# Kernel tuning notes

Measured on AMD Instinct MI355X. Metric: run time of the kernel, lower is better.

## Reference

```python
import jax, jax.numpy as jnp
import numpy as np
from jax import lax

B, NPG = 128, 1024          # graphs, nodes per graph
N = B * NPG                  # total nodes
AVG_DEG = 8
E = N * AVG_DEG              # total edges
F_N, F_E = 128, 32           # node / edge feature dims
LATENT = [32, 32, 32, 1]
D = sum(LATENT)              # total_latent_dim = 97
K = 30                       # sort-pooling k
C1, C2, KW2 = 16, 32, 5      # conv1d channels / kernel
OUT = 2
DENSE = ((K - 2) // 2 + 1 - KW2 + 1) * C2  # 352


def setup_inputs() -> dict:
    key = jax.random.key(0)
    ks = jax.random.split(key, 12)
    inp = {}
    inp["node_feat"] = jax.random.normal(ks[0], (N, F_N), jnp.float32)
    inp["edge_feat"] = jax.random.normal(ks[1], (E, F_E), jnp.float32)
    inp["edge_index"] = jax.random.randint(ks[2], (2, E), 0, N)
    dims = [F_N + F_E] + LATENT
    for i in range(4):
        inp[f"W{i}"] = jax.random.normal(ks[3 + i], (dims[i], dims[i + 1]), jnp.float32) * 0.05
        inp[f"b{i}"] = jnp.zeros((dims[i + 1],), jnp.float32)
    inp["w_conv1"] = jax.random.normal(ks[7], (C1, 1, D), jnp.float32) * 0.05
    inp["b_conv1"] = jnp.zeros((C1,), jnp.float32)
    inp["w_conv2"] = jax.random.normal(ks[8], (C2, C1, KW2), jnp.float32) * 0.05
    inp["b_conv2"] = jnp.zeros((C2,), jnp.float32)
    inp["w_out"] = jax.random.normal(ks[9], (DENSE, OUT), jnp.float32) * 0.05
    inp["b_out"] = jnp.zeros((OUT,), jnp.float32)
    return inp


def _maxpool2(x):
    # MaxPool1d(2, 2) over last axis of [B, C, L]
    return lax.reduce_window(x, -jnp.inf, lax.max, (1, 1, 2), (1, 1, 2), "VALID")


def _forward(node_feat, edge_feat, W0, b0, W1, b1, W2, b2, W3, b3,
             w_conv1, b_conv1, w_conv2, b_conv2, w_out, b_out, edge_index):
    src, dst = edge_index[0], edge_index[1]
    # degree with self-loop, as in DGCNN (divide by deg after linear)
    deg = jnp.ones((N,), node_feat.dtype).at[dst].add(1.0)
    # e2npool: sum incident edge features onto destination nodes
    e2n = jax.ops.segment_sum(edge_feat, dst, num_segments=N)
    cur = jnp.concatenate([node_feat, e2n], axis=1)  # [N, F_N+F_E]
    hops = []
    for W, b in ((W0, b0), (W1, b1), (W2, b2), (W3, b3)):
        # (A + I) X  -> Linear -> / deg -> tanh
        pooled = jax.ops.segment_sum(cur[src], dst, num_segments=N) + cur
        cur = jnp.tanh((pooled @ W + b) / deg[:, None])
        hops.append(cur)
    feat = jnp.concatenate(hops, axis=1).reshape(B, NPG, D)  # [B, NPG, 97]
    # SortPooling: top-k nodes per graph by last latent channel
    _, idx = lax.top_k(feat[:, :, -1], K)                    # [B, K]
    sp = jnp.take_along_axis(feat, idx[:, :, None], axis=1)  # [B, K, D]
    x = sp.reshape(B, 1, K * D)
    x = lax.conv_general_dilated(x, w_conv1, (D,), "VALID",
                                 dimension_numbers=("NCH", "OIH", "NCH"))
    x = jax.nn.relu(x + b_conv1[None, :, None])  # [B, 16, 30]
    x = _maxpool2(x)                              # [B, 16, 15]
    x = lax.conv_general_dilated(x, w_conv2, (1,), "VALID",
                                 dimension_numbers=("NCH", "OIH", "NCH"))
    x = jax.nn.relu(x + b_conv2[None, :, None])  # [B, 32, 11]
    x = x.reshape(B, -1)                          # [B, 352]
    return jax.nn.relu(x @ w_out + b_out)         # [B, OUT]


def reference(node_feat, edge_feat, edge_index, W0, b0, W1, b1, W2, b2, W3, b3,
              w_conv1, b_conv1, w_conv2, b_conv2, w_out, b_out):
    return _forward(node_feat, edge_feat, W0, b0, W1, b1, W2, b2, W3, b3,
                    w_conv1, b_conv1, w_conv2, b_conv2, w_out, b_out, edge_index)
```

## Files before the change

### kernel.cpp

```cpp
#include <hip/hip_runtime.h>
#include <hip/hip_bf16.h>
#include <math.h>

#define N_NODES 131072
#define N_EDGES 1048576
#define B_GR    128
#define NPG_    1024
#define KTOP    30


__global__ __launch_bounds__(256) void k_zero(int* cnt) {
    int i = blockIdx.x * 256 + threadIdx.x;
    if (i < N_NODES) cnt[i] = 0;
}

__global__ __launch_bounds__(256) void k_count(const int* __restrict__ dst, int* __restrict__ cnt) {
    int xcd = blockIdx.x & 7;
    int base = (blockIdx.x >> 3) * 4096 + threadIdx.x;
    #pragma unroll
    for (int it = 0; it < 16; ++it) {
        int e = base + it * 256;
        int d = __builtin_nontemporal_load(dst + e);
        if ((d >> 14) == xcd) atomicAdd(&cnt[d], 1);
    }
}

__global__ __launch_bounds__(256) void k_scan1(const int* __restrict__ cnt,
                                               int* __restrict__ row_start,
                                               int* __restrict__ blocksum) {
    __shared__ int s[256];
    int t = threadIdx.x;
    int i = blockIdx.x * 256 + t;
    int v = cnt[i];
    s[t] = v; __syncthreads();
    for (int o = 1; o < 256; o <<= 1) {
        int x = (t >= o) ? s[t - o] : 0;
        __syncthreads();
        s[t] += x;
        __syncthreads();
    }
    row_start[i] = s[t] - v;
    if (t == 255) blocksum[blockIdx.x] = s[t];
}

__global__ __launch_bounds__(512) void k_scan2(int* __restrict__ blocksum) {
    __shared__ int s[512];
    int t = threadIdx.x;
    int v = blocksum[t];
    s[t] = v; __syncthreads();
    for (int o = 1; o < 512; o <<= 1) {
        int x = (t >= o) ? s[t - o] : 0;
        __syncthreads();
        s[t] += x;
        __syncthreads();
    }
    blocksum[t] = s[t] - v;
}

__global__ __launch_bounds__(256) void k_scan3(int* __restrict__ row_start,
                                               const int* __restrict__ blocksum,
                                               int* __restrict__ cursor) {
    int i = blockIdx.x * 256 + threadIdx.x;
    int r = row_start[i] + blocksum[blockIdx.x];
    row_start[i] = r;
    cursor[i] = r;
}

__global__ __launch_bounds__(256) void k_fill(const int* __restrict__ src,
                                              const int* __restrict__ dst,
                                              int* __restrict__ cursor,
                                              int* __restrict__ csr_src,
                                              int* __restrict__ csr_eid) {
    int xcd = blockIdx.x & 7;
    int base = (blockIdx.x >> 3) * 4096 + threadIdx.x;
    #pragma unroll
    for (int it = 0; it < 16; ++it) {
        int e = base + it * 256;
        int d = __builtin_nontemporal_load(dst + e);
        if ((d >> 14) == xcd) {
            int s = __builtin_nontemporal_load(src + e);
            int pos = atomicAdd(&cursor[d], 1);
            csr_src[pos] = s;
            csr_eid[pos] = e;
        }
    }
}


__global__ __launch_bounds__(256) void k_esum(const float* __restrict__ ef,
                                              const int* __restrict__ row_start,
                                              const int* __restrict__ cnt,
                                              const int* __restrict__ csr_eid,
                                              float* __restrict__ esum) {
    int g = threadIdx.x >> 5, j = threadIdx.x & 31;
    int n0 = (blockIdx.x * 8 + g) * 4;
    int st[4], ln[4];
    #pragma unroll
    for (int i = 0; i < 4; ++i) { st[i] = row_start[n0 + i]; ln[i] = cnt[n0 + i]; }
    float acc[4] = {0.f, 0.f, 0.f, 0.f};
    int base = 0;
    while ((ln[0] > base) | (ln[1] > base) | (ln[2] > base) | (ln[3] > base)) {
        int eid[4][8];
        #pragma unroll
        for (int i = 0; i < 4; ++i) {
            #pragma unroll
            for (int s = 0; s < 8; ++s) {
                int idx = base + s;
                int a = st[i] + ((idx < ln[i]) ? idx : 0);
                a = (a < N_EDGES) ? a : 0;
                eid[i][s] = csr_eid[a];
            }
        }
        #pragma unroll
        for (int i = 0; i < 4; ++i) {
            #pragma unroll
            for (int s = 0; s < 8; ++s) {
                float v = ef[(size_t)eid[i][s] * 32 + j];
                acc[i] += ((base + s) < ln[i]) ? v : 0.f;
            }
        }
        base += 8;
    }
    #pragma unroll
    for (int i = 0; i < 4; ++i)
        esum[(size_t)(n0 + i) * 32 + j] = acc[i];
}


__global__ __launch_bounds__(256) void k_gemm160(const float* __restrict__ nf,
                                                 const float* __restrict__ esum,
                                                 const float* __restrict__ W0,
                                                 float* __restrict__ z0) {
    __shared__ float a[64 * 161];
    int tid = threadIdx.x;
    int n0 = blockIdx.x * 64;
    const float* nfb = nf + (size_t)n0 * 128;
    for (int f = tid; f < 8192; f += 256) {
        int n = f >> 7, k = f & 127;
        a[n * 161 + k] = nfb[f];
    }
    const float* esb = esum + (size_t)n0 * 32;
    for (int f = tid; f < 2048; f += 256) {
        int n = f >> 5, k = f & 31;
        a[n * 161 + 128 + k] = esb[f];
    }
    __syncthreads();
    int wv = __builtin_amdgcn_readfirstlane(tid >> 6);
    int lane = tid & 63;
    int c0 = wv * 8;
    float acc[8] = {0.f, 0.f, 0.f, 0.f, 0.f, 0.f, 0.f, 0.f};
    const float* ar = a + lane * 161;
    for (int k = 0; k < 160; ++k) {
        float av = ar[k];
        #pragma unroll
        for (int jj = 0; jj < 8; ++jj)
            acc[jj] += av * W0[k * 32 + c0 + jj];
    }
    float* zr = z0 + (size_t)(n0 + lane) * 32 + c0;
    *(float4*)zr = make_float4(acc[0], acc[1], acc[2], acc[3]);
    *(float4*)(zr + 4) = make_float4(acc[4], acc[5], acc[6], acc[7]);
}


__global__ __launch_bounds__(256) void k_layer(const float* __restrict__ zin,
                                               const int* __restrict__ row_start,
                                               const int* __restrict__ cnt,
                                               const int* __restrict__ csr_src,
                                               const float* __restrict__ bias,
                                               const float* __restrict__ Wn,
                                               float* __restrict__ hout,
                                               float* __restrict__ znext) {
    __shared__ float Ws[1024];
    int tid = threadIdx.x;
    for (int f = tid; f < 1024; f += 256) Ws[f] = Wn[f];
    __syncthreads();
    int g = tid >> 5, j = tid & 31;
    int n0 = (blockIdx.x * 8 + g) * 4;
    int st[4], ln[4];
    #pragma unroll
    for (int i = 0; i < 4; ++i) { st[i] = row_start[n0 + i]; ln[i] = cnt[n0 + i]; }
    float acc[4];
    #pragma unroll
    for (int i = 0; i < 4; ++i) acc[i] = zin[(size_t)(n0 + i) * 32 + j];
    int base = 0;
    while ((ln[0] > base) | (ln[1] > base) | (ln[2] > base) | (ln[3] > base)) {
        int sid[4][8];
        #pragma unroll
        for (int i = 0; i < 4; ++i) {
            #pragma unroll
            for (int s = 0; s < 8; ++s) {
                int idx = base + s;
                int a = st[i] + ((idx < ln[i]) ? idx : 0);
                a = (a < N_EDGES) ? a : 0;
                sid[i][s] = csr_src[a];
            }
        }
        #pragma unroll
        for (int i = 0; i < 4; ++i) {
            #pragma unroll
            for (int s = 0; s < 8; ++s) {
                float v = zin[(size_t)sid[i][s] * 32 + j];
                acc[i] += ((base + s) < ln[i]) ? v : 0.f;
            }
        }
        base += 8;
    }
    float bj = bias[j];
    float h[4];
    #pragma unroll
    for (int i = 0; i < 4; ++i) {
        float deg = 1.f + (float)ln[i];
        h[i] = tanhf((acc[i] + bj) / deg);
        hout[(size_t)(n0 + i) * 32 + j] = h[i];
    }
    float z[4] = {0.f, 0.f, 0.f, 0.f};
    for (int k = 0; k < 32; ++k) {
        float w = Ws[k * 32 + j];
        #pragma unroll
        for (int i = 0; i < 4; ++i)
            z[i] += __shfl(h[i], k, 32) * w;
    }
    #pragma unroll
    for (int i = 0; i < 4; ++i)
        znext[(size_t)(n0 + i) * 32 + j] = z[i];
}


__global__ __launch_bounds__(256) void k_layer3(const float* __restrict__ zin,
                                                const int* __restrict__ row_start,
                                                const int* __restrict__ cnt,
                                                const int* __restrict__ csr_src,
                                                const float* __restrict__ bias,
                                                const float* __restrict__ W3,
                                                float* __restrict__ hout,
                                                float* __restrict__ z3) {
    int g = threadIdx.x >> 5, j = threadIdx.x & 31;
    int n0 = (blockIdx.x * 8 + g) * 4;
    int st[4], ln[4];
    #pragma unroll
    for (int i = 0; i < 4; ++i) { st[i] = row_start[n0 + i]; ln[i] = cnt[n0 + i]; }
    float acc[4];
    #pragma unroll
    for (int i = 0; i < 4; ++i) acc[i] = zin[(size_t)(n0 + i) * 32 + j];
    int base = 0;
    while ((ln[0] > base) | (ln[1] > base) | (ln[2] > base) | (ln[3] > base)) {
        int sid[4][8];
        #pragma unroll
        for (int i = 0; i < 4; ++i) {
            #pragma unroll
            for (int s = 0; s < 8; ++s) {
                int idx = base + s;
                int a = st[i] + ((idx < ln[i]) ? idx : 0);
                a = (a < N_EDGES) ? a : 0;
                sid[i][s] = csr_src[a];
            }
        }
        #pragma unroll
        for (int i = 0; i < 4; ++i) {
            #pragma unroll
            for (int s = 0; s < 8; ++s) {
                float v = zin[(size_t)sid[i][s] * 32 + j];
                acc[i] += ((base + s) < ln[i]) ? v : 0.f;
            }
        }
        base += 8;
    }
    float bj = bias[j];
    float w3 = W3[j];
    #pragma unroll
    for (int i = 0; i < 4; ++i) {
        float deg = 1.f + (float)ln[i];
        float h = tanhf((acc[i] + bj) / deg);
        hout[(size_t)(n0 + i) * 32 + j] = h;
        float t = h * w3;
        #pragma unroll
        for (int o = 16; o; o >>= 1) t += __shfl_xor(t, o, 32);
        if (j == 0) z3[n0 + i] = t;
    }
}


__global__ __launch_bounds__(256) void k_g3(const float* __restrict__ z3,
                                            const int* __restrict__ row_start,
                                            const int* __restrict__ cnt,
                                            const int* __restrict__ csr_src,
                                            const float* __restrict__ b3,
                                            float* __restrict__ val) {
    int n = blockIdx.x * 256 + threadIdx.x;
    int start = row_start[n], len = cnt[n];
    const int* cs = csr_src + start;
    float s = z3[n];
    int i = 0;
    for (; i + 4 <= len; i += 4)
        s += z3[cs[i]] + z3[cs[i + 1]] + z3[cs[i + 2]] + z3[cs[i + 3]];
    for (; i < len; ++i) s += z3[cs[i]];
    float deg = 1.f + (float)len;
    val[n] = tanhf((s + b3[0]) / deg);
}


__global__ __launch_bounds__(256) void k_head(const float* __restrict__ h0,
                                              const float* __restrict__ h1,
                                              const float* __restrict__ h2,
                                              const float* __restrict__ val,
                                              const float* __restrict__ wc1,
                                              const float* __restrict__ bc1,
                                              const float* __restrict__ wc2,
                                              const float* __restrict__ bc2,
                                              const float* __restrict__ wout,
                                              const float* __restrict__ bout,
                                              float* __restrict__ out) {
    __shared__ float vals[1024];
    __shared__ int selidx[KTOP];
    __shared__ float sp[KTOP * 97];
    __shared__ float y1[16 * 30];
    __shared__ float pool[16 * 15];
    __shared__ float y2[352];
    int b = blockIdx.x, tid = threadIdx.x;
    const float* vb = val + (size_t)b * NPG_;
    for (int u = tid; u < NPG_; u += 256) vals[u] = vb[u];
    __syncthreads();
    if (tid < 64) {
        unsigned long long keys[16];
        #pragma unroll
        for (int r = 0; r < 16; ++r) {
            int u = tid * 16 + r;
            unsigned int bb = __float_as_uint(vals[u]);
            unsigned int ord = (bb & 0x80000000u) ? ~bb : (bb | 0x80000000u);
            keys[r] = ((unsigned long long)ord << 32) |
                      (unsigned long long)(0xFFFFFFFFu - (unsigned int)u);
        }
        for (int k = 0; k < KTOP; ++k) {
            unsigned long long m = keys[0];
            #pragma unroll
            for (int r = 1; r < 16; ++r) m = (keys[r] > m) ? keys[r] : m;
            #pragma unroll
            for (int o = 32; o; o >>= 1) {
                unsigned long long t = __shfl_xor(m, o);
                m = (t > m) ? t : m;
            }
            int u = (int)(0xFFFFFFFFu - (unsigned int)(m & 0xFFFFFFFFull));
            if (tid == 0) selidx[k] = u;
            #pragma unroll
            for (int r = 0; r < 16; ++r)
                if (tid * 16 + r == u) keys[r] = 0ull;
        }
    }
    __syncthreads();
    size_t nb = (size_t)b * NPG_;
    for (int idx = tid; idx < KTOP * 32; idx += 256) {
        int t = idx >> 5, d = idx & 31;
        size_t s = (nb + (size_t)selidx[t]) * 32;
        sp[t * 97 + d]      = h0[s + d];
        sp[t * 97 + 32 + d] = h1[s + d];
        sp[t * 97 + 64 + d] = h2[s + d];
    }
    if (tid < KTOP) sp[tid * 97 + 96] = vb[selidx[tid]];
    __syncthreads();
    for (int idx = tid; idx < 480; idx += 256) {
        int t = idx >> 4, c = idx & 15;
        float acc = bc1[c];
        for (int d = 0; d < 97; ++d) acc += sp[t * 97 + d] * wc1[c * 97 + d];
        y1[c * 30 + t] = fmaxf(acc, 0.f);
    }
    __syncthreads();
    for (int idx = tid; idx < 240; idx += 256) {
        int c = idx / 15, u = idx - c * 15;
        pool[c * 15 + u] = fmaxf(y1[c * 30 + 2 * u], y1[c * 30 + 2 * u + 1]);
    }
    __syncthreads();
    for (int idx = tid; idx < 352; idx += 256) {
        int o = idx / 11, t = idx - o * 11;
        float acc = bc2[o];
        for (int i = 0; i < 16; ++i)
            for (int kk = 0; kk < 5; ++kk)
                acc += pool[i * 15 + t + kk] * wc2[(o * 16 + i) * 5 + kk];
        y2[idx] = fmaxf(acc, 0.f);
    }
    __syncthreads();
    if (tid < 2) {
        float acc = bout[tid];
        for (int m = 0; m < 352; ++m) acc += y2[m] * wout[m * 2 + tid];
        out[b * 2 + tid] = fmaxf(acc, 0.f);
    }
}


extern "C" void kernel_launch(void* const* d_in, const int* in_sizes, int n_in,
                              void* d_out, int out_size, void* d_ws, size_t ws_size,
                              hipStream_t stream) {
    const float* node_feat = (const float*)d_in[0];
    const float* edge_feat = (const float*)d_in[1];
    const int*   eidx      = (const int*)d_in[2];
    const float* W0 = (const float*)d_in[3];
    const float* b0 = (const float*)d_in[4];
    const float* W1 = (const float*)d_in[5];
    const float* b1 = (const float*)d_in[6];
    const float* W2 = (const float*)d_in[7];
    const float* b2 = (const float*)d_in[8];
    const float* W3 = (const float*)d_in[9];
    const float* b3 = (const float*)d_in[10];
    const float* wc1 = (const float*)d_in[11];
    const float* bc1 = (const float*)d_in[12];
    const float* wc2 = (const float*)d_in[13];
    const float* bc2 = (const float*)d_in[14];
    const float* wout = (const float*)d_in[15];
    const float* bout = (const float*)d_in[16];
    float* out = (float*)d_out;

    const int* src = eidx;
    const int* dst = eidx + N_EDGES;

    char* ws = (char*)d_ws;
    size_t off = 0;
    auto alloc = [&](size_t bytes) -> char* {
        char* p = ws + off;
        off += (bytes + 255) & ~(size_t)255;
        return p;
    };
    int* cnt       = (int*)alloc((size_t)N_NODES * 4);
    int* row_start = (int*)alloc((size_t)N_NODES * 4);
    int* cursor    = (int*)alloc((size_t)N_NODES * 4);
    int* blocksum  = (int*)alloc(512 * 4);
    int* csr_src   = (int*)alloc((size_t)N_EDGES * 4);
    int* csr_eid   = (int*)alloc((size_t)N_EDGES * 4);
    float* esum    = (float*)alloc((size_t)N_NODES * 32 * 4);
    float* z0      = (float*)alloc((size_t)N_NODES * 32 * 4);
    float* z1      = (float*)alloc((size_t)N_NODES * 32 * 4);
    float* z2      = (float*)alloc((size_t)N_NODES * 32 * 4);
    float* h0      = (float*)alloc((size_t)N_NODES * 32 * 4);
    float* h1      = (float*)alloc((size_t)N_NODES * 32 * 4);
    float* h2      = (float*)alloc((size_t)N_NODES * 32 * 4);
    float* z3      = (float*)alloc((size_t)N_NODES * 4);
    float* val     = (float*)alloc((size_t)N_NODES * 4);
    (void)ws_size;

    k_zero<<<N_NODES / 256, 256, 0, stream>>>(cnt);
    k_count<<<2048, 256, 0, stream>>>(dst, cnt);
    k_scan1<<<N_NODES / 256, 256, 0, stream>>>(cnt, row_start, blocksum);
    k_scan2<<<1, 512, 0, stream>>>(blocksum);
    k_scan3<<<N_NODES / 256, 256, 0, stream>>>(row_start, blocksum, cursor);
    k_fill<<<2048, 256, 0, stream>>>(src, dst, cursor, csr_src, csr_eid);
    k_esum<<<N_NODES / 32, 256, 0, stream>>>(edge_feat, row_start, cnt, csr_eid, esum);
    k_gemm160<<<N_NODES / 64, 256, 0, stream>>>(node_feat, esum, W0, z0);
    k_layer<<<N_NODES / 32, 256, 0, stream>>>(z0, row_start, cnt, csr_src, b0, W1, h0, z1);
    k_layer<<<N_NODES / 32, 256, 0, stream>>>(z1, row_start, cnt, csr_src, b1, W2, h1, z2);
    k_layer3<<<N_NODES / 32, 256, 0, stream>>>(z2, row_start, cnt, csr_src, b2, W3, h2, z3);
    k_g3<<<N_NODES / 256, 256, 0, stream>>>(z3, row_start, cnt, csr_src, b3, val);
    k_head<<<B_GR, 256, 0, stream>>>(h0, h1, h2, val, wc1, bc1, wc2, bc2, wout, bout, out);
}
```

Before: 582.2 us.

## Fuse CSR build into cooperative kernel, shuffle-broadcast neighbor ids, reorder layer GEMM

The six CSR-construction kernels (zero, count, three scan phases, fill) become one cooperative kernel of 1024 blocks that separates phases with grid.sync, removing several launches. The gather kernels load up to 32 neighbor indices per warp in one coalesced read and broadcast them with __shfl, rather than each lane re-reading the index array. The layer kernels now aggregate the previous h first and apply the 32x32 weight afterwards, which removes the z1/z2 intermediate buffers. Cooperative launch limits occupancy and adds grid-wide barriers, and neighbors beyond 32 take a slower serial path.

```diff
diff --git a/kernel.cpp b/kernel.cpp
--- a/kernel.cpp
+++ b/kernel.cpp
@@ -1,6 +1,9 @@
 #include <hip/hip_runtime.h>
 #include <hip/hip_bf16.h>
+#include <hip/hip_cooperative_groups.h>
 #include <math.h>
+
+namespace cg = cooperative_groups;
 
 #define N_NODES 131072
 #define N_EDGES 1048576
@@ -8,83 +11,91 @@
 #define NPG_    1024
 #define KTOP    30
 
-
-__global__ __launch_bounds__(256) void k_zero(int* cnt) {
-    int i = blockIdx.x * 256 + threadIdx.x;
-    if (i < N_NODES) cnt[i] = 0;
-}
-
-__global__ __launch_bounds__(256) void k_count(const int* __restrict__ dst, int* __restrict__ cnt) {
-    int xcd = blockIdx.x & 7;
-    int base = (blockIdx.x >> 3) * 4096 + threadIdx.x;
-    #pragma unroll
-    for (int it = 0; it < 16; ++it) {
-        int e = base + it * 256;
-        int d = __builtin_nontemporal_load(dst + e);
-        if ((d >> 14) == xcd) atomicAdd(&cnt[d], 1);
-    }
-}
-
-__global__ __launch_bounds__(256) void k_scan1(const int* __restrict__ cnt,
+__global__ __launch_bounds__(256) void k_build(const int* __restrict__ src,
+                                               const int* __restrict__ dst,
+                                               int* __restrict__ cnt,
                                                int* __restrict__ row_start,
-                                               int* __restrict__ blocksum) {
+                                               int* __restrict__ cursor,
+                                               int* __restrict__ blocksum,
+                                               int* __restrict__ csr_src,
+                                               int* __restrict__ csr_eid) {
+    cg::grid_group grid = cg::this_grid();
     __shared__ int s[256];
-    int t = threadIdx.x;
-    int i = blockIdx.x * 256 + t;
-    int v = cnt[i];
-    s[t] = v; __syncthreads();
-    for (int o = 1; o < 256; o <<= 1) {
-        int x = (t >= o) ? s[t - o] : 0;
-        __syncthreads();
-        s[t] += x;
-        __syncthreads();
-    }
-    row_start[i] = s[t] - v;
-    if (t == 255) blocksum[blockIdx.x] = s[t];
-}
-
-__global__ __launch_bounds__(512) void k_scan2(int* __restrict__ blocksum) {
-    __shared__ int s[512];
-    int t = threadIdx.x;
-    int v = blocksum[t];
-    s[t] = v; __syncthreads();
-    for (int o = 1; o < 512; o <<= 1) {
-        int x = (t >= o) ? s[t - o] : 0;
-        __syncthreads();
-        s[t] += x;
-        __syncthreads();
-    }
-    blocksum[t] = s[t] - v;
-}
-
-__global__ __launch_bounds__(256) void k_scan3(int* __restrict__ row_start,
-                                               const int* __restrict__ blocksum,
-                                               int* __restrict__ cursor) {
-    int i = blockIdx.x * 256 + threadIdx.x;
-    int r = row_start[i] + blocksum[blockIdx.x];
-    row_start[i] = r;
-    cursor[i] = r;
-}
-
-__global__ __launch_bounds__(256) void k_fill(const int* __restrict__ src,
-                                              const int* __restrict__ dst,
-                                              int* __restrict__ cursor,
-                                              int* __restrict__ csr_src,
-                                              int* __restrict__ csr_eid) {
-    int xcd = blockIdx.x & 7;
-    int base = (blockIdx.x >> 3) * 4096 + threadIdx.x;
-    #pragma unroll
-    for (int it = 0; it < 16; ++it) {
-        int e = base + it * 256;
-        int d = __builtin_nontemporal_load(dst + e);
-        if ((d >> 14) == xcd) {
-            int s = __builtin_nontemporal_load(src + e);
-            int pos = atomicAdd(&cursor[d], 1);
-            csr_src[pos] = s;
-            csr_eid[pos] = e;
-        }
-    }
-}
+    int tid = threadIdx.x, bid = blockIdx.x;
+
+    {
+        int i = bid * 256 + tid;
+        if (i < N_NODES) cnt[i] = 0;
+    }
+    grid.sync();
+
+    {
+        int xcd = bid & 7;
+        int base = (bid >> 3) * 8192 + tid;
+        #pragma unroll 4
+        for (int it = 0; it < 32; ++it) {
+            int e = base + it * 256;
+            int d = __builtin_nontemporal_load(dst + e);
+            if ((d >> 14) == xcd) atomicAdd(&cnt[d], 1);
+        }
+    }
+    grid.sync();
+
+    if (bid < 512) {
+        int i = bid * 256 + tid;
+        int v = cnt[i];
+        s[tid] = v; __syncthreads();
+        for (int o = 1; o < 256; o <<= 1) {
+            int x = (tid >= o) ? s[tid - o] : 0;
+            __syncthreads();
+            s[tid] += x;
+            __syncthreads();
+        }
+        row_start[i] = s[tid] - v;
+        if (tid == 255) blocksum[bid] = s[tid];
+    }
+    grid.sync();
+
+    if (bid == 0) {
+        int a = blocksum[2 * tid], b = blocksum[2 * tid + 1];
+        int p = a + b;
+        s[tid] = p; __syncthreads();
+        for (int o = 1; o < 256; o <<= 1) {
+            int x = (tid >= o) ? s[tid - o] : 0;
+            __syncthreads();
+            s[tid] += x;
+            __syncthreads();
+        }
+        int excl = s[tid] - p;
+        blocksum[2 * tid] = excl;
+        blocksum[2 * tid + 1] = excl + a;
+    }
+    grid.sync();
+
+    if (bid < 512) {
+        int i = bid * 256 + tid;
+        int r = row_start[i] + blocksum[bid];
+        row_start[i] = r;
+        cursor[i] = r;
+    }
+    grid.sync();
+
+    {
+        int xcd = bid & 7;
+        int base = (bid >> 3) * 8192 + tid;
+        for (int it = 0; it < 32; ++it) {
+            int e = base + it * 256;
+            int d = __builtin_nontemporal_load(dst + e);
+            if ((d >> 14) == xcd) {
+                int sv = __builtin_nontemporal_load(src + e);
+                int pos = atomicAdd(&cursor[d], 1);
+                csr_src[pos] = sv;
+                csr_eid[pos] = e;
+            }
+        }
+    }
+}
+
 
 
 __global__ __launch_bounds__(256) void k_esum(const float* __restrict__ ef,
@@ -94,32 +105,33 @@
                                               float* __restrict__ esum) {
     int g = threadIdx.x >> 5, j = threadIdx.x & 31;
     int n0 = (blockIdx.x * 8 + g) * 4;
-    int st[4], ln[4];
+    int st[4], ln[4], idv[4];
     #pragma unroll
     for (int i = 0; i < 4; ++i) { st[i] = row_start[n0 + i]; ln[i] = cnt[n0 + i]; }
+    #pragma unroll
+    for (int i = 0; i < 4; ++i) {
+        int a = st[i] + ((j < ln[i]) ? j : 0);
+        idv[i] = csr_eid[(a < N_EDGES) ? a : 0];
+    }
     float acc[4] = {0.f, 0.f, 0.f, 0.f};
-    int base = 0;
-    while ((ln[0] > base) | (ln[1] > base) | (ln[2] > base) | (ln[3] > base)) {
-        int eid[4][8];
+    #pragma unroll
+    for (int base = 0; base < 32; base += 8) {
+        if (!((ln[0] > base) | (ln[1] > base) | (ln[2] > base) | (ln[3] > base))) break;
         #pragma unroll
         for (int i = 0; i < 4; ++i) {
             #pragma unroll
-            for (int s = 0; s < 8; ++s) {
-                int idx = base + s;
-                int a = st[i] + ((idx < ln[i]) ? idx : 0);
-                a = (a < N_EDGES) ? a : 0;
-                eid[i][s] = csr_eid[a];
+            for (int s2 = 0; s2 < 8; ++s2) {
+                int sid = __shfl(idv[i], base + s2, 32);
+                float v = ef[(size_t)sid * 32 + j];
+                acc[i] += ((base + s2) < ln[i]) ? v : 0.f;
             }
         }
-        #pragma unroll
-        for (int i = 0; i < 4; ++i) {
-            #pragma unroll
-            for (int s = 0; s < 8; ++s) {
-                float v = ef[(size_t)eid[i][s] * 32 + j];
-                acc[i] += ((base + s) < ln[i]) ? v : 0.f;
-            }
-        }
-        base += 8;
+    }
+    int mx = max(max(ln[0], ln[1]), max(ln[2], ln[3]));
+    for (int idx = 32; idx < mx; ++idx) {
+        #pragma unroll
+        for (int i = 0; i < 4; ++i)
+            if (idx < ln[i]) acc[i] += ef[(size_t)csr_eid[st[i] + idx] * 32 + j];
     }
     #pragma unroll
     for (int i = 0; i < 4; ++i)
@@ -162,115 +174,165 @@
 }
 
 
-__global__ __launch_bounds__(256) void k_layer(const float* __restrict__ zin,
-                                               const int* __restrict__ row_start,
-                                               const int* __restrict__ cnt,
-                                               const int* __restrict__ csr_src,
-                                               const float* __restrict__ bias,
-                                               const float* __restrict__ Wn,
-                                               float* __restrict__ hout,
-                                               float* __restrict__ znext) {
-    __shared__ float Ws[1024];
-    int tid = threadIdx.x;
-    for (int f = tid; f < 1024; f += 256) Ws[f] = Wn[f];
-    __syncthreads();
-    int g = tid >> 5, j = tid & 31;
-    int n0 = (blockIdx.x * 8 + g) * 4;
-    int st[4], ln[4];
-    #pragma unroll
-    for (int i = 0; i < 4; ++i) { st[i] = row_start[n0 + i]; ln[i] = cnt[n0 + i]; }
-    float acc[4];
-    #pragma unroll
-    for (int i = 0; i < 4; ++i) acc[i] = zin[(size_t)(n0 + i) * 32 + j];
-    int base = 0;
-    while ((ln[0] > base) | (ln[1] > base) | (ln[2] > base) | (ln[3] > base)) {
-        int sid[4][8];
-        #pragma unroll
-        for (int i = 0; i < 4; ++i) {
-            #pragma unroll
-            for (int s = 0; s < 8; ++s) {
-                int idx = base + s;
-                int a = st[i] + ((idx < ln[i]) ? idx : 0);
-                a = (a < N_EDGES) ? a : 0;
-                sid[i][s] = csr_src[a];
-            }
-        }
-        #pragma unroll
-        for (int i = 0; i < 4; ++i) {
-            #pragma unroll
-            for (int s = 0; s < 8; ++s) {
-                float v = zin[(size_t)sid[i][s] * 32 + j];
-                acc[i] += ((base + s) < ln[i]) ? v : 0.f;
-            }
-        }
-        base += 8;
-    }
-    float bj = bias[j];
-    float h[4];
-    #pragma unroll
-    for (int i = 0; i < 4; ++i) {
-        float deg = 1.f + (float)ln[i];
-        h[i] = tanhf((acc[i] + bj) / deg);
-        hout[(size_t)(n0 + i) * 32 + j] = h[i];
-    }
-    float z[4] = {0.f, 0.f, 0.f, 0.f};
-    for (int k = 0; k < 32; ++k) {
-        float w = Ws[k * 32 + j];
-        #pragma unroll
-        for (int i = 0; i < 4; ++i)
-            z[i] += __shfl(h[i], k, 32) * w;
-    }
-    #pragma unroll
-    for (int i = 0; i < 4; ++i)
-        znext[(size_t)(n0 + i) * 32 + j] = z[i];
-}
-
-
-__global__ __launch_bounds__(256) void k_layer3(const float* __restrict__ zin,
+__global__ __launch_bounds__(256) void k_layerA(const float* __restrict__ zin,
                                                 const int* __restrict__ row_start,
                                                 const int* __restrict__ cnt,
                                                 const int* __restrict__ csr_src,
                                                 const float* __restrict__ bias,
+                                                float* __restrict__ hout) {
+    int g = threadIdx.x >> 5, j = threadIdx.x & 31;
+    int n0 = (blockIdx.x * 8 + g) * 4;
+    int st[4], ln[4], idv[4];
+    #pragma unroll
+    for (int i = 0; i < 4; ++i) { st[i] = row_start[n0 + i]; ln[i] = cnt[n0 + i]; }
+    #pragma unroll
+    for (int i = 0; i < 4; ++i) {
+        int a = st[i] + ((j < ln[i]) ? j : 0);
+        idv[i] = csr_src[(a < N_EDGES) ? a : 0];
+    }
+    float acc[4];
+    #pragma unroll
+    for (int i = 0; i < 4; ++i) acc[i] = zin[(size_t)(n0 + i) * 32 + j];
+    #pragma unroll
+    for (int base = 0; base < 32; base += 8) {
+        if (!((ln[0] > base) | (ln[1] > base) | (ln[2] > base) | (ln[3] > base))) break;
+        #pragma unroll
+        for (int i = 0; i < 4; ++i) {
+            #pragma unroll
+            for (int s2 = 0; s2 < 8; ++s2) {
+                int sid = __shfl(idv[i], base + s2, 32);
+                float v = zin[(size_t)sid * 32 + j];
+                acc[i] += ((base + s2) < ln[i]) ? v : 0.f;
+            }
+        }
+    }
+    int mx = max(max(ln[0], ln[1]), max(ln[2], ln[3]));
+    for (int idx = 32; idx < mx; ++idx) {
+        #pragma unroll
+        for (int i = 0; i < 4; ++i)
+            if (idx < ln[i]) acc[i] += zin[(size_t)csr_src[st[i] + idx] * 32 + j];
+    }
+    float bj = bias[j];
+    #pragma unroll
+    for (int i = 0; i < 4; ++i)
+        hout[(size_t)(n0 + i) * 32 + j] = tanhf((acc[i] + bj) / (1.f + (float)ln[i]));
+}
+
+
+__global__ __launch_bounds__(256) void k_layerB(const float* __restrict__ hin,
+                                                const int* __restrict__ row_start,
+                                                const int* __restrict__ cnt,
+                                                const int* __restrict__ csr_src,
+                                                const float* __restrict__ bias,
+                                                const float* __restrict__ Wn,
+                                                float* __restrict__ hout) {
+    __shared__ float Ws[1024];
+    int tid = threadIdx.x;
+    for (int f = tid; f < 1024; f += 256) Ws[f] = Wn[f];
+    __syncthreads();
+    int g = tid >> 5, j = tid & 31;
+    int n0 = (blockIdx.x * 8 + g) * 4;
+    int st[4], ln[4], idv[4];
+    #pragma unroll
+    for (int i = 0; i < 4; ++i) { st[i] = row_start[n0 + i]; ln[i] = cnt[n0 + i]; }
+    #pragma unroll
+    for (int i = 0; i < 4; ++i) {
+        int a = st[i] + ((j < ln[i]) ? j : 0);
+        idv[i] = csr_src[(a < N_EDGES) ? a : 0];
+    }
+    float acc[4];
+    #pragma unroll
+    for (int i = 0; i < 4; ++i) acc[i] = hin[(size_t)(n0 + i) * 32 + j];
+    #pragma unroll
+    for (int base = 0; base < 32; base += 8) {
+        if (!((ln[0] > base) | (ln[1] > base) | (ln[2] > base) | (ln[3] > base))) break;
+        #pragma unroll
+        for (int i = 0; i < 4; ++i) {
+            #pragma unroll
+            for (int s2 = 0; s2 < 8; ++s2) {
+                int sid = __shfl(idv[i], base + s2, 32);
+                float v = hin[(size_t)sid * 32 + j];
+                acc[i] += ((base + s2) < ln[i]) ? v : 0.f;
+            }
+        }
+    }
+    int mx = max(max(ln[0], ln[1]), max(ln[2], ln[3]));
+    for (int idx = 32; idx < mx; ++idx) {
+        #pragma unroll
+        for (int i = 0; i < 4; ++i)
+            if (idx < ln[i]) acc[i] += hin[(size_t)csr_src[st[i] + idx] * 32 + j];
+    }
+    float y[4] = {0.f, 0.f, 0.f, 0.f};
+    for (int k = 0; k < 32; ++k) {
+        float w = Ws[k * 32 + j];
+        #pragma unroll
+        for (int i = 0; i < 4; ++i)
+            y[i] += __shfl(acc[i], k, 32) * w;
+    }
+    float bj = bias[j];
+    #pragma unroll
+    for (int i = 0; i < 4; ++i)
+        hout[(size_t)(n0 + i) * 32 + j] = tanhf((y[i] + bj) / (1.f + (float)ln[i]));
+}
+
+
+__global__ __launch_bounds__(256) void k_layerC(const float* __restrict__ hin,
+                                                const int* __restrict__ row_start,
+                                                const int* __restrict__ cnt,
+                                                const int* __restrict__ csr_src,
+                                                const float* __restrict__ bias,
+                                                const float* __restrict__ Wn,
                                                 const float* __restrict__ W3,
                                                 float* __restrict__ hout,
                                                 float* __restrict__ z3) {
-    int g = threadIdx.x >> 5, j = threadIdx.x & 31;
+    __shared__ float Ws[1024];
+    int tid = threadIdx.x;
+    for (int f = tid; f < 1024; f += 256) Ws[f] = Wn[f];
+    __syncthreads();
+    int g = tid >> 5, j = tid & 31;
     int n0 = (blockIdx.x * 8 + g) * 4;
-    int st[4], ln[4];
+    int st[4], ln[4], idv[4];
     #pragma unroll
     for (int i = 0; i < 4; ++i) { st[i] = row_start[n0 + i]; ln[i] = cnt[n0 + i]; }
+    #pragma unroll
+    for (int i = 0; i < 4; ++i) {
+        int a = st[i] + ((j < ln[i]) ? j : 0);
+        idv[i] = csr_src[(a < N_EDGES) ? a : 0];
+    }
     float acc[4];
     #pragma unroll
-    for (int i = 0; i < 4; ++i) acc[i] = zin[(size_t)(n0 + i) * 32 + j];
-    int base = 0;
-    while ((ln[0] > base) | (ln[1] > base) | (ln[2] > base) | (ln[3] > base)) {
-        int sid[4][8];
+    for (int i = 0; i < 4; ++i) acc[i] = hin[(size_t)(n0 + i) * 32 + j];
+    #pragma unroll
+    for (int base = 0; base < 32; base += 8) {
+        if (!((ln[0] > base) | (ln[1] > base) | (ln[2] > base) | (ln[3] > base))) break;
         #pragma unroll
         for (int i = 0; i < 4; ++i) {
             #pragma unroll
-            for (int s = 0; s < 8; ++s) {
-                int idx = base + s;
-                int a = st[i] + ((idx < ln[i]) ? idx : 0);
-                a = (a < N_EDGES) ? a : 0;
-                sid[i][s] = csr_src[a];
+            for (int s2 = 0; s2 < 8; ++s2) {
+                int sid = __shfl(idv[i], base + s2, 32);
+                float v = hin[(size_t)sid * 32 + j];
+                acc[i] += ((base + s2) < ln[i]) ? v : 0.f;
             }
         }
-        #pragma unroll
-        for (int i = 0; i < 4; ++i) {
-            #pragma unroll
-            for (int s = 0; s < 8; ++s) {
-                float v = zin[(size_t)sid[i][s] * 32 + j];
-                acc[i] += ((base + s) < ln[i]) ? v : 0.f;
-            }
-        }
-        base += 8;
+    }
+    int mx = max(max(ln[0], ln[1]), max(ln[2], ln[3]));
+    for (int idx = 32; idx < mx; ++idx) {
+        #pragma unroll
+        for (int i = 0; i < 4; ++i)
+            if (idx < ln[i]) acc[i] += hin[(size_t)csr_src[st[i] + idx] * 32 + j];
+    }
+    float y[4] = {0.f, 0.f, 0.f, 0.f};
+    for (int k = 0; k < 32; ++k) {
+        float w = Ws[k * 32 + j];
+        #pragma unroll
+        for (int i = 0; i < 4; ++i)
+            y[i] += __shfl(acc[i], k, 32) * w;
     }
     float bj = bias[j];
     float w3 = W3[j];
     #pragma unroll
     for (int i = 0; i < 4; ++i) {
-        float deg = 1.f + (float)ln[i];
-        float h = tanhf((acc[i] + bj) / deg);
+        float h = tanhf((y[i] + bj) / (1.f + (float)ln[i]));
         hout[(size_t)(n0 + i) * 32 + j] = h;
         float t = h * w3;
         #pragma unroll
@@ -426,8 +488,6 @@
     int* csr_eid   = (int*)alloc((size_t)N_EDGES * 4);
     float* esum    = (float*)alloc((size_t)N_NODES * 32 * 4);
     float* z0      = (float*)alloc((size_t)N_NODES * 32 * 4);
-    float* z1      = (float*)alloc((size_t)N_NODES * 32 * 4);
-    float* z2      = (float*)alloc((size_t)N_NODES * 32 * 4);
     float* h0      = (float*)alloc((size_t)N_NODES * 32 * 4);
     float* h1      = (float*)alloc((size_t)N_NODES * 32 * 4);
     float* h2      = (float*)alloc((size_t)N_NODES * 32 * 4);
@@ -435,17 +495,17 @@
     float* val     = (float*)alloc((size_t)N_NODES * 4);
     (void)ws_size;
 
-    k_zero<<<N_NODES / 256, 256, 0, stream>>>(cnt);
-    k_count<<<2048, 256, 0, stream>>>(dst, cnt);
-    k_scan1<<<N_NODES / 256, 256, 0, stream>>>(cnt, row_start, blocksum);
-    k_scan2<<<1, 512, 0, stream>>>(blocksum);
-    k_scan3<<<N_NODES / 256, 256, 0, stream>>>(row_start, blocksum, cursor);
-    k_fill<<<2048, 256, 0, stream>>>(src, dst, cursor, csr_src, csr_eid);
+    {
+        void* args[] = {(void*)&src, (void*)&dst, (void*)&cnt, (void*)&row_start,
+                        (void*)&cursor, (void*)&blocksum, (void*)&csr_src, (void*)&csr_eid};
+        hipLaunchCooperativeKernel((const void*)k_build, dim3(1024), dim3(256),
+                                   args, 0, stream);
+    }
     k_esum<<<N_NODES / 32, 256, 0, stream>>>(edge_feat, row_start, cnt, csr_eid, esum);
     k_gemm160<<<N_NODES / 64, 256, 0, stream>>>(node_feat, esum, W0, z0);
-    k_layer<<<N_NODES / 32, 256, 0, stream>>>(z0, row_start, cnt, csr_src, b0, W1, h0, z1);
-    k_layer<<<N_NODES / 32, 256, 0, stream>>>(z1, row_start, cnt, csr_src, b1, W2, h1, z2);
-    k_layer3<<<N_NODES / 32, 256, 0, stream>>>(z2, row_start, cnt, csr_src, b2, W3, h2, z3);
+    k_layerA<<<N_NODES / 32, 256, 0, stream>>>(z0, row_start, cnt, csr_src, b0, h0);
+    k_layerB<<<N_NODES / 32, 256, 0, stream>>>(h0, row_start, cnt, csr_src, b1, W1, h1);
+    k_layerC<<<N_NODES / 32, 256, 0, stream>>>(h1, row_start, cnt, csr_src, b2, W2, W3, h2, z3);
     k_g3<<<N_NODES / 256, 256, 0, stream>>>(z3, row_start, cnt, csr_src, b3, val);
     k_head<<<B_GR, 256, 0, stream>>>(h0, h1, h2, val, wc1, bc1, wc2, bc2, wout, bout, out);
 }
```

Result: slower. 1.041 ms (+78.8%).
